# Kernel tuning notes

Hardware: AMD Instinct MI355X
Metric: run time of the kernel (lower is better)

The kernel has to match this reference:

```python
import jax, jax.numpy as jnp
import numpy as np

N_NODES = 50000
N_EDGES = 800000
IN_F, E_F, OUT_F = 128, 32, 128

def setup_inputs() -> dict:
    key = jax.random.key(0)
    ks = jax.random.split(key, 8)
    return {
        "h": jax.random.normal(ks[0], (N_NODES, IN_F), dtype=jnp.float32),
        "eftr": jax.random.normal(ks[1], (N_EDGES, E_F), dtype=jnp.float32),
        "weight": jax.random.normal(ks[2], (IN_F + E_F, OUT_F), dtype=jnp.float32) * (1.0 / np.sqrt(IN_F + E_F)),
        "W_w": jax.random.normal(ks[3], (OUT_F, IN_F + OUT_F), dtype=jnp.float32) * (1.0 / np.sqrt(IN_F + OUT_F)),
        "W_b": jax.random.normal(ks[4], (OUT_F,), dtype=jnp.float32) * 0.01,
        "bias": jnp.zeros((OUT_F,), dtype=jnp.float32),
        "src_idx": jax.random.randint(ks[5], (N_EDGES,), 0, N_NODES, dtype=jnp.int64) if jax.config.jax_enable_x64 else jax.random.randint(ks[5], (N_EDGES,), 0, N_NODES, dtype=jnp.int32),
        "dst_idx": jax.random.randint(ks[6], (N_EDGES,), 0, N_NODES, dtype=jnp.int32),
        "num_dst": N_NODES,
    }

def reference(h, eftr, weight, W_w, W_b, bias, src_idx, dst_idx, num_dst):
    # Segment-mean of concat([h[src], eftr]) over dst neighborhoods.
    # Sum node part and edge part separately (avoids materializing the concat mailbox).
    sum_h = jax.ops.segment_sum(h[src_idx], dst_idx, num_segments=num_dst)   # [D, IN_F]
    sum_e = jax.ops.segment_sum(eftr, dst_idx, num_segments=num_dst)        # [D, E_F]
    cnt = jax.ops.segment_sum(jnp.ones((dst_idx.shape[0],), h.dtype), dst_idx, num_segments=num_dst)
    denom = jnp.maximum(cnt, 1.0)[:, None]  # zero-degree nodes -> h_neigh = 0
    feat_mean = jnp.concatenate([sum_h / denom, sum_e / denom], axis=-1)    # [D, IN_F+E_F]
    h_neigh = feat_mean @ weight                                            # [D, OUT_F]
    h_dst = h[:num_dst]
    h_prime = jnp.concatenate([h_dst, h_neigh], axis=1) @ W_w.T + W_b       # Linear W
    h_prime = h_prime + bias
    return h_prime
```

## Files before the change

kernel.cpp:

```cpp
#include <hip/hip_runtime.h>

#define NN   50000
#define NE   800000
#define INF  128
#define EF   32
#define OUTF 128
#define NBLK ((NN + 1023) / 1024)
#define CVT_BLKS 3125

typedef __attribute__((ext_vector_type(8))) short     short8;
typedef __attribute__((ext_vector_type(8))) unsigned short ushort8;
typedef __attribute__((ext_vector_type(4))) float     float4v;
typedef __attribute__((ext_vector_type(2))) float     float2v;

__device__ __forceinline__ unsigned short f2bf(float f) {
    union { float f; unsigned int u; } c; c.f = f;
    const unsigned int r = (c.u + 0x7FFFu + ((c.u >> 16) & 1u)) >> 16;
    return (unsigned short)r;
}

__global__ void pack_kernel(const float* __restrict__ weight,
                            const float* __restrict__ W_w,
                            unsigned short* __restrict__ Mb) {
    __shared__ float wrow[32][129];
    __shared__ float wcol[16][129];
    const int b = blockIdx.x;
    const int kb = b >> 3;
    const int ct = b & 7;
    const int lane = threadIdx.x;
    const int colLoc = lane & 15;
    const int quad = lane >> 4;
    const int col = ct * 16 + colLoc;

    ushort8 v;
    if (kb < 4) {
        const int k0 = kb * 32 + quad * 8;
        const float4 p0 = *(const float4*)(W_w + (size_t)col * 256 + k0);
        const float4 p1 = *(const float4*)(W_w + (size_t)col * 256 + k0 + 4);
        v[0] = f2bf(p0.x); v[1] = f2bf(p0.y); v[2] = f2bf(p0.z); v[3] = f2bf(p0.w);
        v[4] = f2bf(p1.x); v[5] = f2bf(p1.y); v[6] = f2bf(p1.z); v[7] = f2bf(p1.w);
    } else {
        const int m0 = (kb - 4) * 32;
        for (int idx = lane; idx < 32 * 128; idx += 64)
            wrow[idx >> 7][idx & 127] =
                weight[(size_t)(m0 + (idx >> 7)) * 128 + (idx & 127)];
        for (int idx = lane; idx < 16 * 128; idx += 64)
            wcol[idx >> 7][idx & 127] =
                W_w[(size_t)(ct * 16 + (idx >> 7)) * 256 + 128 + (idx & 127)];
        __syncthreads();
        float acc[8] = {};
        for (int c = 0; c < 128; ++c) {
            const float wc = wcol[colLoc][c];
#pragma unroll
            for (int i = 0; i < 8; ++i)
                acc[i] += wrow[quad * 8 + i][c] * wc;
        }
#pragma unroll
        for (int i = 0; i < 8; ++i) v[i] = f2bf(acc[i]);
    }
    *(ushort8*)(Mb + ((size_t)(b * 64 + lane) * 8)) = v;
}

__global__ __launch_bounds__(256)
void cvt_hist_kernel(const float* __restrict__ h,
                     unsigned short* __restrict__ hb,
                     const int* __restrict__ dst,
                     int* __restrict__ off,
                     int* __restrict__ rank) {
    const int b = blockIdx.x;
    if (b < CVT_BLKS) {
        const size_t i = (size_t)(b * 256 + threadIdx.x) * 8;
        const float4 a0 = *(const float4*)(h + i);
        const float4 a1 = *(const float4*)(h + i + 4);
        ushort8 v;
        v[0] = f2bf(a0.x); v[1] = f2bf(a0.y); v[2] = f2bf(a0.z); v[3] = f2bf(a0.w);
        v[4] = f2bf(a1.x); v[5] = f2bf(a1.y); v[6] = f2bf(a1.z); v[7] = f2bf(a1.w);
        *(ushort8*)(hb + i) = v;
        return;
    }
    if (b == CVT_BLKS) {
        if (threadIdx.x < 16) {
            ushort8 z = {};
            *(ushort8*)(hb + (size_t)NN * INF + threadIdx.x * 8) = z;
        }
        return;
    }
    const int e = ((b - CVT_BLKS - 1) * 256 + threadIdx.x) * 4;
    if (e < NE) {
        const int4 d = *(const int4*)(dst + e);
        int4 r;
        r.x = atomicAdd(&off[d.x], 1);
        r.y = atomicAdd(&off[d.y], 1);
        r.z = atomicAdd(&off[d.z], 1);
        r.w = atomicAdd(&off[d.w], 1);
        *(int4*)(rank + e) = r;
    }
}

__global__ __launch_bounds__(256)
void scan1_kernel(const int* __restrict__ off, int* __restrict__ partial) {
    const int b = blockIdx.x;
    const int tid = threadIdx.x;
    const int idx = b * 1024 + tid * 4;
    int v0 = 0, v1 = 0, v2 = 0, v3 = 0;
    if (idx + 3 < NN) {
        const int4 q = *(const int4*)(off + idx);
        v0 = q.x; v1 = q.y; v2 = q.z; v3 = q.w;
    } else {
        if (idx + 0 < NN) v0 = off[idx + 0];
        if (idx + 1 < NN) v1 = off[idx + 1];
        if (idx + 2 < NN) v2 = off[idx + 2];
    }
    int t = v0 + v1 + v2 + v3;
#pragma unroll
    for (int ofs = 32; ofs > 0; ofs >>= 1) t += __shfl_down(t, ofs);
    __shared__ int wsum[4];
    if ((tid & 63) == 0) wsum[tid >> 6] = t;
    __syncthreads();
    if (tid == 0) partial[b] = wsum[0] + wsum[1] + wsum[2] + wsum[3];
}

__global__ __launch_bounds__(256)
void scan3_kernel(int* __restrict__ off, const int* __restrict__ partial) {
    __shared__ int blockbase;
    __shared__ int wsum[4];
    const int b = blockIdx.x;
    const int tid = threadIdx.x;
    const int lane = tid & 63;
    const int wid = tid >> 6;

    if (b == 0 && tid == 0) off[NN] = NE;

    if (wid == 0) {
        const int v = (lane < NBLK) ? partial[lane] : 0;
        int x = v;
#pragma unroll
        for (int ofs = 1; ofs < 64; ofs <<= 1) {
            const int t = __shfl_up(x, ofs);
            if (lane >= ofs) x += t;
        }
        if (lane == b) blockbase = x - v;
    }

    const int idx = b * 1024 + tid * 4;
    int v0 = 0, v1 = 0, v2 = 0, v3 = 0;
    if (idx + 3 < NN) {
        const int4 q = *(const int4*)(off + idx);
        v0 = q.x; v1 = q.y; v2 = q.z; v3 = q.w;
    } else {
        if (idx + 0 < NN) v0 = off[idx + 0];
        if (idx + 1 < NN) v1 = off[idx + 1];
        if (idx + 2 < NN) v2 = off[idx + 2];
    }
    const int tsum = v0 + v1 + v2 + v3;
    int x = tsum;
#pragma unroll
    for (int ofs = 1; ofs < 64; ofs <<= 1) {
        const int t = __shfl_up(x, ofs);
        if (lane >= ofs) x += t;
    }
    if (lane == 63) wsum[wid] = x;
    __syncthreads();
    int wp = 0;
    for (int w = 0; w < wid; ++w) wp += wsum[w];
    const int base = blockbase + wp + (x - tsum);
    if (idx + 0 < NN) off[idx + 0] = base;
    if (idx + 1 < NN) off[idx + 1] = base + v0;
    if (idx + 2 < NN) off[idx + 2] = base + v0 + v1;
    if (idx + 3 < NN) off[idx + 3] = base + v0 + v1 + v2;
}

__global__ __launch_bounds__(256)
void scatter_ids_kernel(const int* __restrict__ srcv,
                        const int* __restrict__ dst,
                        const int* __restrict__ off,
                        const int* __restrict__ rank,
                        int2* __restrict__ eo2) {
    const int e = (blockIdx.x * 256 + threadIdx.x) * 4;
    if (e < NE) {
        const int4 s = *(const int4*)(srcv + e);
        const int4 d = *(const int4*)(dst + e);
        const int4 r = *(const int4*)(rank + e);
        eo2[off[d.x] + r.x] = make_int2(s.x, e + 0);
        eo2[off[d.y] + r.y] = make_int2(s.y, e + 1);
        eo2[off[d.z] + r.z] = make_int2(s.z, e + 2);
        eo2[off[d.w] + r.w] = make_int2(s.w, e + 3);
    }
}

__global__ __launch_bounds__(256)
void gather_kernel(const unsigned short* __restrict__ hb,
                   const float* __restrict__ eftr,
                   const int* __restrict__ off,
                   const int2* __restrict__ eo2,
                   unsigned short* __restrict__ mean_h,
                   unsigned short* __restrict__ mean_e) {
    const int tid = threadIdx.x;
    const int lane = tid & 63;
    const int node = blockIdx.x * 4 + (tid >> 6);
    if (node >= NN) return;

    const int start = off[node];
    const int end   = off[node + 1];

    const int ql = lane & 15;
    const int qg = lane >> 4;

    float ax[8] = {0.f, 0.f, 0.f, 0.f, 0.f, 0.f, 0.f, 0.f};
    float aex = 0.f, aey = 0.f;

    for (int j = start; j < end; j += 16) {
#pragma unroll
        for (int u = 0; u < 4; ++u) {
            const int eidx = j + u * 4 + qg;
            const bool valid = eidx < end;
            const int2 se = eo2[valid ? eidx : (end - 1)];
            const int s = valid ? se.x : NN;
            const int e = se.y;

            const uint4 hv = *(const uint4*)(hb + (size_t)s * INF + ql * 8);
#pragma unroll
            for (int k = 0; k < 4; ++k) {
                const unsigned w = (&hv.x)[k];
                union { unsigned u; float f; } lo, hi;
                lo.u = w << 16;
                hi.u = w & 0xffff0000u;
                ax[2 * k]     += lo.f;
                ax[2 * k + 1] += hi.f;
            }

            const float2v ev = __builtin_nontemporal_load(
                (const float2v*)(eftr + (size_t)e * EF + ql * 2));
            aex += valid ? ev.x : 0.f;
            aey += valid ? ev.y : 0.f;
        }
    }

#pragma unroll
    for (int k = 0; k < 8; ++k) {
        ax[k] += __shfl_xor(ax[k], 16);
        ax[k] += __shfl_xor(ax[k], 32);
    }
    aex += __shfl_xor(aex, 16); aex += __shfl_xor(aex, 32);
    aey += __shfl_xor(aey, 16); aey += __shfl_xor(aey, 32);

    if (qg == 0) {
        const float inv = 1.f / fmaxf((float)(end - start), 1.f);
        ushort8 mv;
#pragma unroll
        for (int k = 0; k < 8; ++k) mv[k] = f2bf(ax[k] * inv);
        *(ushort8*)(mean_h + (size_t)node * INF + ql * 8) = mv;
        const unsigned me =
            (unsigned)f2bf(aex * inv) | ((unsigned)f2bf(aey * inv) << 16);
        *(unsigned*)(mean_e + (size_t)node * EF + ql * 2) = me;
    }
}

__global__ __launch_bounds__(256)
void node_gemm_kernel(const unsigned short* __restrict__ hb,
                      const unsigned short* __restrict__ mean_h,
                      const unsigned short* __restrict__ mean_e,
                      const unsigned short* __restrict__ Mb,
                      const float* __restrict__ W_b,
                      const float* __restrict__ bias,
                      float* __restrict__ out) {
    const int tid = threadIdx.x;
    const int lane = tid & 63;
    const int wid = tid >> 6;
    const int nt = blockIdx.x * 4 + wid;
    const int m16 = lane & 15;
    const int quad = lane >> 4;
    const int koff = quad * 8;

    const int anode = nt * 16 + m16;
    const int nclamp = (anode < NN) ? anode : (NN - 1);

    float4v acc[8] = {};

    for (int kb = 0; kb < 9; ++kb) {
        const unsigned short* srcp;
        if (kb < 4)
            srcp = hb + (size_t)nclamp * INF + kb * 32 + koff;
        else if (kb < 8)
            srcp = mean_h + (size_t)nclamp * INF + (kb - 4) * 32 + koff;
        else
            srcp = mean_e + (size_t)nclamp * EF + koff;
        const short8 a = *(const short8*)(const void*)srcp;

        const short8* bp = (const short8*)(Mb + (size_t)kb * 8 * 64 * 8);
#pragma unroll
        for (int ct = 0; ct < 8; ++ct) {
            const short8 b = bp[ct * 64 + lane];
            acc[ct] = __builtin_amdgcn_mfma_f32_16x16x32_bf16(a, b, acc[ct], 0, 0, 0);
        }
    }

    float cv[8];
#pragma unroll
    for (int ct = 0; ct < 8; ++ct) {
        const int c = ct * 16 + m16;
        cv[ct] = W_b[c] + bias[c];
    }

#pragma unroll
    for (int r = 0; r < 4; ++r) {
        const int nrow = nt * 16 + quad * 4 + r;
        if (nrow < NN) {
            float* orow = out + (size_t)nrow * OUTF;
#pragma unroll
            for (int ct = 0; ct < 8; ++ct)
                __builtin_nontemporal_store(acc[ct][r] + cv[ct],
                                            &orow[ct * 16 + m16]);
        }
    }
}

extern "C" void kernel_launch(void* const* d_in, const int* in_sizes, int n_in,
                              void* d_out, int out_size, void* d_ws, size_t ws_size,
                              hipStream_t stream) {
    const float* h      = (const float*)d_in[0];
    const float* eftr   = (const float*)d_in[1];
    const float* weight = (const float*)d_in[2];
    const float* W_w    = (const float*)d_in[3];
    const float* W_b    = (const float*)d_in[4];
    const float* bias   = (const float*)d_in[5];
    const int*   src    = (const int*)d_in[6];
    const int*   dst    = (const int*)d_in[7];
    float* out = (float*)d_out;

    char* base = (char*)d_ws;
    unsigned short* mean_h = (unsigned short*)(base);
    unsigned short* mean_e = (unsigned short*)(base + 12800000);
    unsigned short* h_bf   = (unsigned short*)(base + 16000000);
    unsigned short* Mb     = (unsigned short*)(base + 28800512);
    int*   off             = (int*)(base + 28874240);
    int2*  eo2             = (int2*)(base + 29074944);
    int*   rank            = (int*)(base + 35474944);
    int*   partial         = (int*)(base + 38674944);

    hipMemsetAsync(off, 0, (size_t)NN * sizeof(int), stream);

    pack_kernel<<<72, 64, 0, stream>>>(weight, W_w, Mb);
    cvt_hist_kernel<<<CVT_BLKS + 1 + (NE / 4 + 255) / 256, 256, 0, stream>>>(
        h, h_bf, dst, off, rank);
    scan1_kernel<<<NBLK, 256, 0, stream>>>(off, partial);
    scan3_kernel<<<NBLK, 256, 0, stream>>>(off, partial);
    scatter_ids_kernel<<<(NE / 4 + 255) / 256, 256, 0, stream>>>(src, dst, off,
                                                                 rank, eo2);
    gather_kernel<<<(NN + 3) / 4, 256, 0, stream>>>(h_bf, eftr, off, eo2,
                                                    mean_h, mean_e);
    node_gemm_kernel<<<(NN / 64) + 1, 256, 0, stream>>>(h_bf, mean_h, mean_e,
                                                        Mb, W_b, bias, out);
}
```

Measured before the change: 302.4 us.

## Restructure gather: wave-wide edge-list load with readlane broadcast, lane-per-column accumulation

The gather kernel now has the whole wavefront load up to 64 edge (src, eid) pairs at once, then broadcasts them with readlane. Each lane accumulates two bf16 columns of the node feature row, so edges are processed 8 at a time and no cross-lane reduction is needed for the node part. Edge features are split across the two half-waves and combined with a single shuffle. This removes the padded zero row in h_bf and the related block in cvt_hist_kernel, because invalid edges are never loaded. In exchange, each edge's feature row is fetched as many narrow 4-byte loads instead of wide per-lane vectors, and the per-edge work is serialized inside the wave.

```diff
diff --git a/kernel.cpp b/kernel.cpp
--- a/kernel.cpp
+++ b/kernel.cpp
@@ -11,7 +11,6 @@
 typedef __attribute__((ext_vector_type(8))) short     short8;
 typedef __attribute__((ext_vector_type(8))) unsigned short ushort8;
 typedef __attribute__((ext_vector_type(4))) float     float4v;
-typedef __attribute__((ext_vector_type(2))) float     float2v;
 
 __device__ __forceinline__ unsigned short f2bf(float f) {
     union { float f; unsigned int u; } c; c.f = f;
@@ -78,14 +77,7 @@
         *(ushort8*)(hb + i) = v;
         return;
     }
-    if (b == CVT_BLKS) {
-        if (threadIdx.x < 16) {
-            ushort8 z = {};
-            *(ushort8*)(hb + (size_t)NN * INF + threadIdx.x * 8) = z;
-        }
-        return;
-    }
-    const int e = ((b - CVT_BLKS - 1) * 256 + threadIdx.x) * 4;
+    const int e = ((b - CVT_BLKS) * 256 + threadIdx.x) * 4;
     if (e < NE) {
         const int4 d = *(const int4*)(dst + e);
         int4 r;
@@ -203,57 +195,66 @@
     const int start = off[node];
     const int end   = off[node + 1];
 
-    const int ql = lane & 15;
-    const int qg = lane >> 4;
-
-    float ax[8] = {0.f, 0.f, 0.f, 0.f, 0.f, 0.f, 0.f, 0.f};
-    float aex = 0.f, aey = 0.f;
-
-    for (int j = start; j < end; j += 16) {
-#pragma unroll
-        for (int u = 0; u < 4; ++u) {
-            const int eidx = j + u * 4 + qg;
-            const bool valid = eidx < end;
-            const int2 se = eo2[valid ? eidx : (end - 1)];
-            const int s = valid ? se.x : NN;
-            const int e = se.y;
-
-            const uint4 hv = *(const uint4*)(hb + (size_t)s * INF + ql * 8);
-#pragma unroll
-            for (int k = 0; k < 4; ++k) {
-                const unsigned w = (&hv.x)[k];
+    float ax = 0.f, ay = 0.f, ae = 0.f;
+    const unsigned short* hcol = hb + lane * 2;
+    const int el = lane & 31;
+    const bool lowhalf = (lane < 32);
+
+    for (int base = start; base < end; base += 64) {
+        const int m = min(64, end - base);
+        int px = 0, py = 0;
+        if (lane < m) {
+            const long long pv =
+                __builtin_nontemporal_load((const long long*)(eo2 + base + lane));
+            px = (int)pv;
+            py = (int)(pv >> 32);
+        }
+        int j = 0;
+        for (; j + 7 < m; j += 8) {
+            int s[8], e[8];
+#pragma unroll
+            for (int u = 0; u < 8; ++u) {
+                s[u] = __builtin_amdgcn_readlane(px, j + u);
+                e[u] = __builtin_amdgcn_readlane(py, j + u);
+            }
+            unsigned v[8];
+#pragma unroll
+            for (int u = 0; u < 8; ++u)
+                v[u] = *(const unsigned*)(hcol + (size_t)s[u] * INF);
+            float f[4];
+#pragma unroll
+            for (int u = 0; u < 4; ++u) {
+                const int ee = lowhalf ? e[2 * u] : e[2 * u + 1];
+                f[u] = __builtin_nontemporal_load(&eftr[(size_t)ee * EF + el]);
+            }
+#pragma unroll
+            for (int u = 0; u < 8; ++u) {
                 union { unsigned u; float f; } lo, hi;
-                lo.u = w << 16;
-                hi.u = w & 0xffff0000u;
-                ax[2 * k]     += lo.f;
-                ax[2 * k + 1] += hi.f;
+                lo.u = v[u] << 16;
+                hi.u = v[u] & 0xffff0000u;
+                ax += lo.f; ay += hi.f;
             }
-
-            const float2v ev = __builtin_nontemporal_load(
-                (const float2v*)(eftr + (size_t)e * EF + ql * 2));
-            aex += valid ? ev.x : 0.f;
-            aey += valid ? ev.y : 0.f;
-        }
-    }
-
-#pragma unroll
-    for (int k = 0; k < 8; ++k) {
-        ax[k] += __shfl_xor(ax[k], 16);
-        ax[k] += __shfl_xor(ax[k], 32);
-    }
-    aex += __shfl_xor(aex, 16); aex += __shfl_xor(aex, 32);
-    aey += __shfl_xor(aey, 16); aey += __shfl_xor(aey, 32);
-
-    if (qg == 0) {
-        const float inv = 1.f / fmaxf((float)(end - start), 1.f);
-        ushort8 mv;
-#pragma unroll
-        for (int k = 0; k < 8; ++k) mv[k] = f2bf(ax[k] * inv);
-        *(ushort8*)(mean_h + (size_t)node * INF + ql * 8) = mv;
-        const unsigned me =
-            (unsigned)f2bf(aex * inv) | ((unsigned)f2bf(aey * inv) << 16);
-        *(unsigned*)(mean_e + (size_t)node * EF + ql * 2) = me;
-    }
+            ae += (f[0] + f[1]) + (f[2] + f[3]);
+        }
+        for (; j < m; ++j) {
+            const int s0 = __builtin_amdgcn_readlane(px, j);
+            const int e0 = __builtin_amdgcn_readlane(py, j);
+            const unsigned v0 = *(const unsigned*)(hcol + (size_t)s0 * INF);
+            union { unsigned u; float f; } lo, hi;
+            lo.u = v0 << 16;
+            hi.u = v0 & 0xffff0000u;
+            ax += lo.f; ay += hi.f;
+            if (lowhalf) ae += __builtin_nontemporal_load(&eftr[(size_t)e0 * EF + el]);
+        }
+    }
+
+    ae += __shfl(ae, lane + 32);
+
+    const float inv = 1.f / fmaxf((float)(end - start), 1.f);
+    const unsigned mx = f2bf(ax * inv);
+    const unsigned my = f2bf(ay * inv);
+    *(unsigned*)(mean_h + (size_t)node * INF + lane * 2) = mx | (my << 16);
+    if (lowhalf) mean_e[(size_t)node * EF + el] = f2bf(ae * inv);
 }
 
 __global__ __launch_bounds__(256)
@@ -332,8 +333,8 @@
     unsigned short* mean_h = (unsigned short*)(base);
     unsigned short* mean_e = (unsigned short*)(base + 12800000);
     unsigned short* h_bf   = (unsigned short*)(base + 16000000);
-    unsigned short* Mb     = (unsigned short*)(base + 28800512);
-    int*   off             = (int*)(base + 28874240);
+    unsigned short* Mb     = (unsigned short*)(base + 28800000);
+    int*   off             = (int*)(base + 28873728);
     int2*  eo2             = (int2*)(base + 29074944);
     int*   rank            = (int*)(base + 35474944);
     int*   partial         = (int*)(base + 38674944);
@@ -341,7 +342,7 @@
     hipMemsetAsync(off, 0, (size_t)NN * sizeof(int), stream);
 
     pack_kernel<<<72, 64, 0, stream>>>(weight, W_w, Mb);
-    cvt_hist_kernel<<<CVT_BLKS + 1 + (NE / 4 + 255) / 256, 256, 0, stream>>>(
+    cvt_hist_kernel<<<CVT_BLKS + (NE / 4 + 255) / 256, 256, 0, stream>>>(
         h, h_bf, dst, off, rank);
     scan1_kernel<<<NBLK, 256, 0, stream>>>(off, partial);
     scan3_kernel<<<NBLK, 256, 0, stream>>>(off, partial);
```

Result: no change. 304.2 us (+0.6%).
